# Optimization experiments

Hardware: AMD Instinct MI355X
Metric: run time of the kernel (lower is better)

The kernel has to match this reference:

```python
import jax, jax.numpy as jnp
import numpy as np

B, S, P, D, H = 2, 4096, 1024, 1024, 16  # batch, byte seq, patches, d_model, heads


def setup_inputs() -> dict:
    key = jax.random.key(0)
    ks = jax.random.split(key, 8)
    init = 0.02
    queries = jax.random.normal(ks[0], (B, S, D), dtype=jnp.float32)
    patch_representations = jax.random.normal(ks[1], (B, P, D), dtype=jnp.float32)
    patch_boundaries = jax.random.randint(ks[2], (B, S), 0, 2, dtype=jnp.int32)
    wq = jax.random.normal(ks[3], (D, D), dtype=jnp.float32) * init
    wk = jax.random.normal(ks[4], (D, D), dtype=jnp.float32) * init
    wv = jax.random.normal(ks[5], (D, D), dtype=jnp.float32) * init
    wo = jax.random.normal(ks[6], (D, D), dtype=jnp.float32) * init
    bq = jnp.zeros((D,), jnp.float32)
    bk = jnp.zeros((D,), jnp.float32)
    bv = jnp.zeros((D,), jnp.float32)
    bo = jnp.zeros((D,), jnp.float32)
    return {"queries": queries, "patch_representations": patch_representations,
            "patch_boundaries": patch_boundaries,
            "wq": wq, "wk": wk, "wv": wv, "wo": wo,
            "bq": bq, "bk": bk, "bv": bv, "bo": bo}


def reference(queries, patch_representations, patch_boundaries,
              wq, wk, wv, wo, bq, bk, bv, bo):
    b, s, d = queries.shape
    p = patch_representations.shape[1]
    h = H
    dh = d // h
    scale = 1.0 / jnp.sqrt(jnp.asarray(dh, queries.dtype))

    # in-projections (torch Linear: x @ W.T + b)
    q = (queries @ wq.T + bq).reshape(b, s, h, dh)
    k = (patch_representations @ wk.T + bk).reshape(b, p, h, dh)
    v = (patch_representations @ wv.T + bv).reshape(b, p, h, dh)

    # scores: [b, h, s, p]
    scores = jnp.einsum('bqhd,bkhd->bhqk', q, k) * scale

    # data-dependent patch-boundary mask: byte t may attend to patch j iff j <= cumsum(boundaries)[t]
    patch_idx = jnp.cumsum(patch_boundaries, axis=1)          # [b, s]
    mask = jnp.arange(p)[None, None, :] > patch_idx[:, :, None]  # [b, s, p], True = masked
    scores = jnp.where(mask[:, None, :, :], jnp.finfo(scores.dtype).min, scores)

    attn = jax.nn.softmax(scores, axis=-1)                    # dropout inactive (eval)
    out = jnp.einsum('bhqk,bkhd->bqhd', attn, v).reshape(b, s, d)
    return out @ wo.T + bo
```

## Files before the change

kernel.cpp:

```cpp
#include <hip/hip_runtime.h>


#define B_ 2
#define S_ 4096
#define P_ 1024
#define D_ 1024
#define H_ 16
#define DH_ 64

#define NCONV 14336

typedef __attribute__((ext_vector_type(8))) short short8;
typedef __attribute__((ext_vector_type(4))) float f32x4;
typedef __attribute__((ext_vector_type(16))) float f32x16;

#define KSCALE 0.18033688011112042f

#if __has_builtin(__builtin_amdgcn_exp2f)
#define EXP2(x) __builtin_amdgcn_exp2f(x)
#else
#define EXP2(x) exp2f(x)
#endif

static __device__ __forceinline__ unsigned short f2bf(float f) {
    unsigned int u = __float_as_uint(f);
    u += 0x7FFFu + ((u >> 16) & 1u);
    return (unsigned short)(u >> 16);
}

static __device__ __forceinline__ unsigned int cvtpk(float lo, float hi) {
    unsigned int r;
    asm("v_cvt_pk_bf16_f32 %0, %1, %2" : "=v"(r) : "v"(lo), "v"(hi));
    return r;
}

static __device__ __forceinline__ void plswap(unsigned int& x, unsigned int& y) {
    asm volatile("v_permlane32_swap_b32 %0, %1" : "+v"(x), "+v"(y));
}

static __device__ __forceinline__ void gll16(const unsigned short* g,
                                             const unsigned short* l) {
    __builtin_amdgcn_global_load_lds(
        (const __attribute__((address_space(1))) unsigned int*)g,
        (__attribute__((address_space(3))) unsigned int*)l,
        16, 0, 0);
}

__global__ __launch_bounds__(256) void xattn_convert_all(
    const float* __restrict__ queries, const float* __restrict__ patches,
    const float* __restrict__ wq, const float* __restrict__ wk,
    const float* __restrict__ wv, const float* __restrict__ wo,
    unsigned short* __restrict__ qb, unsigned short* __restrict__ pb,
    unsigned short* __restrict__ wqb, unsigned short* __restrict__ wkb,
    unsigned short* __restrict__ wvb, unsigned short* __restrict__ wob,
    const int* __restrict__ bounds, int* __restrict__ pidx) {
    if (blockIdx.x >= NCONV) {
        __shared__ int sdata[256];
        int b = blockIdx.x - NCONV;
        int t = threadIdx.x;
        const int* src = bounds + b * S_ + t * 16;
        int vals[16];
        int run = 0;
#pragma unroll
        for (int i = 0; i < 16; ++i) { run += src[i]; vals[i] = run; }
        sdata[t] = run;
        __syncthreads();
        for (int off = 1; off < 256; off <<= 1) {
            int v = (t >= off) ? sdata[t - off] : 0;
            __syncthreads();
            sdata[t] += v;
            __syncthreads();
        }
        int prefix = (t > 0) ? sdata[t - 1] : 0;
        int* dst = pidx + b * S_ + t * 16;
#pragma unroll
        for (int i = 0; i < 16; ++i) dst[i] = prefix + vals[i];
        return;
    }
    const int NQ = (B_ * S_ * D_) / 4;
    const int NP = (B_ * P_ * D_) / 4;
    const int NW = (D_ * D_) / 4;
    int i = blockIdx.x * 256 + threadIdx.x;
    const float* src;
    unsigned short* dst;
    int j;
    if (i < NQ) { src = queries; dst = qb; j = i; }
    else if (i < NQ + NP) { src = patches; dst = pb; j = i - NQ; }
    else {
        int k = i - NQ - NP;
        int wsel = k >> 18;
        j = k & (NW - 1);
        if (wsel == 0) { src = wq; dst = wqb; }
        else if (wsel == 1) { src = wk; dst = wkb; }
        else if (wsel == 2) { src = wv; dst = wvb; }
        else { src = wo; dst = wob; }
    }
    float4 v = ((const float4*)src)[j];
    ushort4 o;
    o.x = f2bf(v.x); o.y = f2bf(v.y); o.z = f2bf(v.z); o.w = f2bf(v.w);
    ((ushort4*)dst)[j] = o;
}

__global__ __launch_bounds__(512) void xattn_gemm_qkv(
    const unsigned short* __restrict__ qb, const unsigned short* __restrict__ pb,
    const unsigned short* __restrict__ wqb, const unsigned short* __restrict__ wkb,
    const unsigned short* __restrict__ wvb,
    const float* __restrict__ bq, const float* __restrict__ bk,
    const float* __restrict__ bv,
    unsigned short* __restrict__ Qout, unsigned short* __restrict__ Kout,
    unsigned short* __restrict__ Vout) {
    const int K = 1024, N = 1024;
    const int byy = blockIdx.y;
    int z, my;
    if (byy < 64)      { z = 0; my = byy; }
    else if (byy < 80) { z = 1; my = byy - 64; }
    else               { z = 2; my = byy - 80; }
    const unsigned short* A = (z == 0) ? qb : pb;
    const unsigned short* W = (z == 0) ? wqb : ((z == 1) ? wkb : wvb);
    const float* bias = (z == 0) ? bq : ((z == 1) ? bk : bv);

    __shared__ unsigned short As[2][128 * 32];
    __shared__ unsigned short Bs[2][256 * 32];

    const int m0 = my * 128;
    const int n0 = blockIdx.x * 256;
    const int t = threadIdx.x;
    const int w = t >> 6;
    const int l = t & 63;
    const int fr = l & 15, fq = l >> 4;
    const int wr = w >> 2, wc = w & 3;

    const int r0s = t >> 2;
    const int csw = ((t & 3) ^ ((t >> 3) & 3)) * 8;
    const unsigned short* Ap0 = A + (size_t)(m0 + r0s) * K + csw;
    const unsigned short* Wp0 = W + (size_t)(n0 + r0s) * K + csw;
    const unsigned short* Wp1 = W + (size_t)(n0 + 128 + r0s) * K + csw;

    const int gsw = (fq ^ ((fr >> 1) & 3)) * 8;

    f32x4 acc[4][4];
#pragma unroll
    for (int i = 0; i < 4; ++i)
#pragma unroll
        for (int j = 0; j < 4; ++j) acc[i][j] = (f32x4){0.f, 0.f, 0.f, 0.f};

    gll16(Ap0, &As[0][w * 512]);
    gll16(Wp0, &Bs[0][w * 512]);
    gll16(Wp1, &Bs[0][4096 + w * 512]);

    for (int kt = 0; kt < 32; ++kt) {
        __builtin_amdgcn_s_barrier();
        if (kt + 1 < 32) {
            const int nb = (kt + 1) & 1;
            const int ks = (kt + 1) * 32;
            gll16(Ap0 + ks, &As[nb][w * 512]);
            gll16(Wp0 + ks, &Bs[nb][w * 512]);
            gll16(Wp1 + ks, &Bs[nb][4096 + w * 512]);
            asm volatile("s_waitcnt vmcnt(3)" ::: "memory");
        } else {
            asm volatile("s_waitcnt vmcnt(0)" ::: "memory");
        }
        __builtin_amdgcn_sched_barrier(0);
        __builtin_amdgcn_s_barrier();

        const unsigned short* Ac = As[kt & 1];
        const unsigned short* Bc = Bs[kt & 1];
        short8 af[4], bf[4];
#pragma unroll
        for (int i = 0; i < 4; ++i)
            af[i] = *(const short8*)&Ac[(wr * 64 + i * 16 + fr) * 32 + gsw];
#pragma unroll
        for (int j = 0; j < 4; ++j)
            bf[j] = *(const short8*)&Bc[(wc * 64 + j * 16 + fr) * 32 + gsw];
        __builtin_amdgcn_s_setprio(1);
#pragma unroll
        for (int i = 0; i < 4; ++i)
#pragma unroll
            for (int j = 0; j < 4; ++j)
                acc[i][j] = __builtin_amdgcn_mfma_f32_16x16x32_bf16(af[i], bf[j], acc[i][j], 0, 0, 0);
        __builtin_amdgcn_s_setprio(0);
    }

#pragma unroll
    for (int j = 0; j < 4; ++j) {
        int n = n0 + wc * 64 + j * 16 + fr;
        float bvv = bias[n];
#pragma unroll
        for (int i = 0; i < 4; ++i) {
            int mbase = m0 + wr * 64 + i * 16 + fq * 4;
#pragma unroll
            for (int r = 0; r < 4; ++r) {
                float val = acc[i][j][r] + bvv;
                int m = mbase + r;
                if (z == 0) {
                    Qout[(size_t)m * N + n] = f2bf(val * KSCALE);
                } else if (z == 1) {
                    int bb = m >> 10, p = m & (P_ - 1);
                    int hh = n >> 6, k = n & 63;
                    size_t base = ((size_t)((bb * H_ + hh) * 16 + (p >> 6))) * 4096;
                    int off = (((p >> 5) & 1) * 4 + (k >> 4)) * 512 +
                              (((k >> 3) & 1) * 32 + (p & 31)) * 8 + (k & 7);
                    Kout[base + off] = f2bf(val);
                } else {
                    int bb = m >> 10, p = m & (P_ - 1);
                    int hh = n >> 6, d = n & 63;
                    size_t base = ((size_t)((bb * H_ + hh) * 16 + (p >> 6))) * 4096;
                    int off = ((d >> 5) * 4 + ((p >> 4) & 3)) * 512 +
                              ((((p >> 3) & 1) * 32) + (d & 31)) * 8 + (p & 7);
                    Vout[base + off] = f2bf(val);
                }
            }
        }
    }
}

__global__ __launch_bounds__(512) void xattn_gemm_o(
    const unsigned short* __restrict__ A,
    const unsigned short* __restrict__ W,
    const float* __restrict__ bias,
    float* __restrict__ Cout) {
    const int K = 1024, N = 1024;
    __shared__ unsigned short As[2][128 * 32];
    __shared__ unsigned short Bs[2][256 * 32];

    const int m0 = blockIdx.y * 128;
    const int n0 = blockIdx.x * 256;
    const int t = threadIdx.x;
    const int w = t >> 6;
    const int l = t & 63;
    const int fr = l & 15, fq = l >> 4;
    const int wr = w >> 2, wc = w & 3;

    const int r0s = t >> 2;
    const int csw = ((t & 3) ^ ((t >> 3) & 3)) * 8;
    const unsigned short* Ap0 = A + (size_t)(m0 + r0s) * K + csw;
    const unsigned short* Wp0 = W + (size_t)(n0 + r0s) * K + csw;
    const unsigned short* Wp1 = W + (size_t)(n0 + 128 + r0s) * K + csw;

    const int gsw = (fq ^ ((fr >> 1) & 3)) * 8;

    f32x4 acc[4][4];
#pragma unroll
    for (int i = 0; i < 4; ++i)
#pragma unroll
        for (int j = 0; j < 4; ++j) acc[i][j] = (f32x4){0.f, 0.f, 0.f, 0.f};

    gll16(Ap0, &As[0][w * 512]);
    gll16(Wp0, &Bs[0][w * 512]);
    gll16(Wp1, &Bs[0][4096 + w * 512]);

    for (int kt = 0; kt < 32; ++kt) {
        __builtin_amdgcn_s_barrier();
        if (kt + 1 < 32) {
            const int nb = (kt + 1) & 1;
            const int ks = (kt + 1) * 32;
            gll16(Ap0 + ks, &As[nb][w * 512]);
            gll16(Wp0 + ks, &Bs[nb][w * 512]);
            gll16(Wp1 + ks, &Bs[nb][4096 + w * 512]);
            asm volatile("s_waitcnt vmcnt(3)" ::: "memory");
        } else {
            asm volatile("s_waitcnt vmcnt(0)" ::: "memory");
        }
        __builtin_amdgcn_sched_barrier(0);
        __builtin_amdgcn_s_barrier();

        const unsigned short* Ac = As[kt & 1];
        const unsigned short* Bc = Bs[kt & 1];
        short8 af[4], bf[4];
#pragma unroll
        for (int i = 0; i < 4; ++i)
            af[i] = *(const short8*)&Ac[(wr * 64 + i * 16 + fr) * 32 + gsw];
#pragma unroll
        for (int j = 0; j < 4; ++j)
            bf[j] = *(const short8*)&Bc[(wc * 64 + j * 16 + fr) * 32 + gsw];
        __builtin_amdgcn_s_setprio(1);
#pragma unroll
        for (int i = 0; i < 4; ++i)
#pragma unroll
            for (int j = 0; j < 4; ++j)
                acc[i][j] = __builtin_amdgcn_mfma_f32_16x16x32_bf16(af[i], bf[j], acc[i][j], 0, 0, 0);
        __builtin_amdgcn_s_setprio(0);
    }

#pragma unroll
    for (int j = 0; j < 4; ++j) {
        int n = n0 + wc * 64 + j * 16 + fr;
        float bvv = bias[n];
#pragma unroll
        for (int i = 0; i < 4; ++i) {
            int mbase = m0 + wr * 64 + i * 16 + fq * 4;
#pragma unroll
            for (int r = 0; r < 4; ++r)
                Cout[(size_t)(mbase + r) * N + n] = acc[i][j][r] + bvv;
        }
    }
}

__global__ __launch_bounds__(512) void xattn_attn_mfma(
    const unsigned short* __restrict__ Qb,
    const unsigned short* __restrict__ Kf,
    const unsigned short* __restrict__ Vf,
    const int* __restrict__ pidx,
    unsigned short* __restrict__ Ob) {
    __shared__ unsigned short Ks[3][4096];
    __shared__ unsigned short Vs[3][4096];

    const int q0 = (31 - blockIdx.x) * 128;
    const int h = blockIdx.y;
    const int b = blockIdx.z;
    const int t = threadIdx.x;
    const int w = t >> 6, l = t & 63;
    const int lq = l & 31, lh = l >> 5;
    const int wq4 = w & 3, role = w >> 2;
    const int qw = q0 + wq4 * 32;

    const unsigned short* qrow =
        Qb + (size_t)(b * S_ + qw + lq) * D_ + h * DH_ + lh * 8;
    short8 qf[4];
#pragma unroll
    for (int ks = 0; ks < 4; ++ks) qf[ks] = *(const short8*)(qrow + ks * 16);

    const int prow = pidx[b * S_ + qw + lq];
    const int limit = pidx[b * S_ + q0 + 127];
    const int ntiles = (min(limit, P_ - 1) + 64) >> 6;
    const int nfull = (pidx[b * S_ + q0] + 1) >> 6;

    float l4[4] = {0.f, 0.f, 0.f, 0.f};
    f32x16 oacc[2] = {{}, {}};

    const unsigned short* kfb =
        Kf + (size_t)((b * H_ + h) * 16) * 4096 + w * 512 + l * 8;
    const unsigned short* vfb =
        Vf + (size_t)((b * H_ + h) * 16) * 4096 + w * 512 + l * 8;

    gll16(kfb, &Ks[0][w * 512]);
    gll16(vfb, &Vs[0][w * 512]);
    if (ntiles > 1) {
        gll16(kfb + 4096, &Ks[1][w * 512]);
        gll16(vfb + 4096, &Vs[1][w * 512]);
    }

    int cur = 0, nx2 = 2;
    for (int kt = 0; kt < ntiles; ++kt) {
        __builtin_amdgcn_s_barrier();
        if (kt + 2 < ntiles) {
            gll16(kfb + (size_t)(kt + 2) * 4096, &Ks[nx2][w * 512]);
            gll16(vfb + (size_t)(kt + 2) * 4096, &Vs[nx2][w * 512]);
            asm volatile("s_waitcnt vmcnt(4)" ::: "memory");
        } else if (kt + 1 < ntiles) {
            asm volatile("s_waitcnt vmcnt(2)" ::: "memory");
        } else {
            asm volatile("s_waitcnt vmcnt(0)" ::: "memory");
        }
        __builtin_amdgcn_sched_barrier(0);

        const unsigned short* Kc = Ks[cur];
        const unsigned short* Vc = Vs[cur];
        const int c0 = kt * 64;

        f32x16 sa = {};
        __builtin_amdgcn_s_setprio(1);
#pragma unroll
        for (int ks = 0; ks < 4; ++ks) {
            short8 kfr = *(const short8*)&Kc[(role * 4 + ks) * 512 + l * 8];
            sa = __builtin_amdgcn_mfma_f32_32x32x16_bf16(kfr, qf[ks], sa, 0, 0, 0);
        }
        __builtin_amdgcn_s_setprio(0);

        if (kt >= nfull) {
#pragma unroll
            for (int r = 0; r < 16; ++r) {
                const int pg = c0 + role * 32 + (r & 3) + 8 * (r >> 2) + 4 * lh;
                float p = EXP2(sa[r]);
                p = (pg > prow) ? 0.f : p;
                sa[r] = p;
                l4[r & 3] += p;
            }
        } else {
#pragma unroll
            for (int r = 0; r < 16; ++r) {
                float p = EXP2(sa[r]);
                sa[r] = p;
                l4[r & 3] += p;
            }
        }

        short8 pa[2];
#pragma unroll
        for (int psl = 0; psl < 2; ++psl) {
            const int rA = psl * 8;
            unsigned int X0 = cvtpk(sa[rA + 0], sa[rA + 1]);
            unsigned int Y0 = cvtpk(sa[rA + 4], sa[rA + 5]);
            unsigned int X1 = cvtpk(sa[rA + 2], sa[rA + 3]);
            unsigned int Y1 = cvtpk(sa[rA + 6], sa[rA + 7]);
            plswap(X0, Y0);
            plswap(X1, Y1);
            uint4 u = {X0, X1, Y0, Y1};
            pa[psl] = *(short8*)&u;
        }

        __builtin_amdgcn_s_setprio(1);
#pragma unroll
        for (int dt = 0; dt < 2; ++dt)
#pragma unroll
            for (int psl = 0; psl < 2; ++psl) {
                short8 vfr = *(const short8*)
                    &Vc[(dt * 4 + role * 2 + psl) * 512 + l * 8];
                oacc[dt] = __builtin_amdgcn_mfma_f32_32x32x16_bf16(pa[psl], vfr, oacc[dt], 0, 0, 0);
            }
        __builtin_amdgcn_s_setprio(0);

        cur = (cur == 2) ? 0 : cur + 1;
        nx2 = (nx2 == 2) ? 0 : nx2 + 1;
    }

    float lsum = (l4[0] + l4[1]) + (l4[2] + l4[3]);
    float* cf = (float*)&Ks[0][0];
    float* lf = (float*)&Vs[0][0];
    const int ci = wq4 * 64 + l;

    __builtin_amdgcn_s_barrier();
    if (role) {
#pragma unroll
        for (int r = 0; r < 16; ++r) cf[ci * 16 + r] = oacc[0][r];
        lf[ci] = lsum;
    }
    __builtin_amdgcn_s_barrier();
    if (!role) {
#pragma unroll
        for (int r = 0; r < 16; ++r) oacc[0][r] += cf[ci * 16 + r];
        lsum += lf[ci];
    }
    __builtin_amdgcn_s_barrier();
    if (role) {
#pragma unroll
        for (int r = 0; r < 16; ++r) cf[ci * 16 + r] = oacc[1][r];
    }
    __builtin_amdgcn_s_barrier();
    if (!role) {
#pragma unroll
        for (int r = 0; r < 16; ++r) oacc[1][r] += cf[ci * 16 + r];

        lsum += __shfl_xor(lsum, 32);
        const float inv = 1.0f / lsum;

        unsigned short* ob = Ob + (size_t)(b * S_ + qw) * D_ + h * DH_;
#pragma unroll
        for (int r = 0; r < 16; ++r) {
            const int qr = (r & 3) + 8 * (r >> 2) + 4 * lh;
            const float invr = __shfl(inv, qr);
            ob[(size_t)qr * D_ + lq] = f2bf(oacc[0][r] * invr);
            ob[(size_t)qr * D_ + 32 + lq] = f2bf(oacc[1][r] * invr);
        }
    }
}

extern "C" void kernel_launch(void* const* d_in, const int* in_sizes, int n_in,
                              void* d_out, int out_size, void* d_ws, size_t ws_size,
                              hipStream_t stream) {
    const float* queries = (const float*)d_in[0];
    const float* patches = (const float*)d_in[1];
    const int* bounds    = (const int*)d_in[2];
    const float* wq = (const float*)d_in[3];
    const float* wk = (const float*)d_in[4];
    const float* wv = (const float*)d_in[5];
    const float* wo = (const float*)d_in[6];
    const float* bq = (const float*)d_in[7];
    const float* bk = (const float*)d_in[8];
    const float* bv = (const float*)d_in[9];
    const float* bo = (const float*)d_in[10];
    float* out = (float*)d_out;

    char* ws = (char*)d_ws;
    unsigned short* qb    = (unsigned short*)(ws + 0);
    unsigned short* pb    = (unsigned short*)(ws + 16777216);
    unsigned short* wqb   = (unsigned short*)(ws + 20971520);
    unsigned short* wkb   = (unsigned short*)(ws + 23068672);
    unsigned short* wvb   = (unsigned short*)(ws + 25165824);
    unsigned short* wob   = (unsigned short*)(ws + 27262976);
    unsigned short* Qbf   = (unsigned short*)(ws + 29360128);
    unsigned short* Kfr   = (unsigned short*)(ws + 46137344);
    unsigned short* Vfr   = (unsigned short*)(ws + 50331648);
    unsigned short* attnb = (unsigned short*)(ws + 54525952);
    int* pidx             = (int*)(ws + 71303168);

    xattn_convert_all<<<dim3(NCONV + B_), 256, 0, stream>>>(
        queries, patches, wq, wk, wv, wo, qb, pb, wqb, wkb, wvb, wob,
        bounds, pidx);
    xattn_gemm_qkv<<<dim3(4, 96), 512, 0, stream>>>(
        qb, pb, wqb, wkb, wvb, bq, bk, bv, Qbf, Kfr, Vfr);
    xattn_attn_mfma<<<dim3(S_ / 128, H_, B_), 512, 0, stream>>>(
        Qbf, Kfr, Vfr, pidx, attnb);
    xattn_gemm_o<<<dim3(4, 64), 512, 0, stream>>>(attnb, wob, bo, out);
}
```

Baseline: 232.6 us.

## Process two KV tiles per iteration with double-buffered LDS in attention

The attention loop now handles pairs of 64-wide K/V tiles per iteration, using two 8192-element LDS buffers instead of three 4096-element ones. Interleaving the score MFMAs and the softmax/PV work for two tiles aims to raise instruction-level parallelism and halve the number of barriers and wait points. In exchange it uses more LDS and registers. When the tile count is odd it also computes one extra tile, which is fully masked to zero.

Result: slower. 251.0 us (+7.9%).

```diff
diff --git a/kernel.cpp b/kernel.cpp
--- a/kernel.cpp
+++ b/kernel.cpp
@@ -302,8 +302,8 @@
     const unsigned short* __restrict__ Vf,
     const int* __restrict__ pidx,
     unsigned short* __restrict__ Ob) {
-    __shared__ unsigned short Ks[3][4096];
-    __shared__ unsigned short Vs[3][4096];
+    __shared__ unsigned short Ks[2][8192];
+    __shared__ unsigned short Vs[2][8192];
 
     const int q0 = (31 - blockIdx.x) * 128;
     const int h = blockIdx.y;
@@ -324,6 +324,7 @@
     const int limit = pidx[b * S_ + q0 + 127];
     const int ntiles = (min(limit, P_ - 1) + 64) >> 6;
     const int nfull = (pidx[b * S_ + q0] + 1) >> 6;
+    const int npairs = (ntiles + 1) >> 1;
 
     float l4[4] = {0.f, 0.f, 0.f, 0.f};
     f32x16 oacc[2] = {{}, {}};
@@ -334,21 +335,22 @@
         Vf + (size_t)((b * H_ + h) * 16) * 4096 + w * 512 + l * 8;
 
     gll16(kfb, &Ks[0][w * 512]);
+    gll16(kfb + 4096, &Ks[0][4096 + w * 512]);
     gll16(vfb, &Vs[0][w * 512]);
-    if (ntiles > 1) {
-        gll16(kfb + 4096, &Ks[1][w * 512]);
-        gll16(vfb + 4096, &Vs[1][w * 512]);
-    }
-
-    int cur = 0, nx2 = 2;
-    for (int kt = 0; kt < ntiles; ++kt) {
+    gll16(vfb + 4096, &Vs[0][4096 + w * 512]);
+
+    for (int p = 0; p < npairs; ++p) {
+        const int cur = p & 1;
         __builtin_amdgcn_s_barrier();
-        if (kt + 2 < ntiles) {
-            gll16(kfb + (size_t)(kt + 2) * 4096, &Ks[nx2][w * 512]);
-            gll16(vfb + (size_t)(kt + 2) * 4096, &Vs[nx2][w * 512]);
+        if (p + 1 < npairs) {
+            const int nb = cur ^ 1;
+            const unsigned short* kn = kfb + (size_t)(2 * p + 2) * 4096;
+            const unsigned short* vn = vfb + (size_t)(2 * p + 2) * 4096;
+            gll16(kn, &Ks[nb][w * 512]);
+            gll16(kn + 4096, &Ks[nb][4096 + w * 512]);
+            gll16(vn, &Vs[nb][w * 512]);
+            gll16(vn + 4096, &Vs[nb][4096 + w * 512]);
             asm volatile("s_waitcnt vmcnt(4)" ::: "memory");
-        } else if (kt + 1 < ntiles) {
-            asm volatile("s_waitcnt vmcnt(2)" ::: "memory");
         } else {
             asm volatile("s_waitcnt vmcnt(0)" ::: "memory");
         }
@@ -356,36 +358,55 @@
 
         const unsigned short* Kc = Ks[cur];
         const unsigned short* Vc = Vs[cur];
-        const int c0 = kt * 64;
-
-        f32x16 sa = {};
+        const int ta = 2 * p, tb = 2 * p + 1;
+
+        f32x16 sa = {}, sb = {};
         __builtin_amdgcn_s_setprio(1);
 #pragma unroll
         for (int ks = 0; ks < 4; ++ks) {
-            short8 kfr = *(const short8*)&Kc[(role * 4 + ks) * 512 + l * 8];
-            sa = __builtin_amdgcn_mfma_f32_32x32x16_bf16(kfr, qf[ks], sa, 0, 0, 0);
+            short8 ka = *(const short8*)&Kc[(role * 4 + ks) * 512 + l * 8];
+            short8 kb = *(const short8*)&Kc[4096 + (role * 4 + ks) * 512 + l * 8];
+            sa = __builtin_amdgcn_mfma_f32_32x32x16_bf16(ka, qf[ks], sa, 0, 0, 0);
+            sb = __builtin_amdgcn_mfma_f32_32x32x16_bf16(kb, qf[ks], sb, 0, 0, 0);
         }
         __builtin_amdgcn_s_setprio(0);
 
-        if (kt >= nfull) {
+        if (ta >= nfull) {
 #pragma unroll
             for (int r = 0; r < 16; ++r) {
-                const int pg = c0 + role * 32 + (r & 3) + 8 * (r >> 2) + 4 * lh;
-                float p = EXP2(sa[r]);
-                p = (pg > prow) ? 0.f : p;
-                sa[r] = p;
-                l4[r & 3] += p;
+                const int pg = ta * 64 + role * 32 + (r & 3) + 8 * (r >> 2) + 4 * lh;
+                float pv = EXP2(sa[r]);
+                pv = (pg > prow) ? 0.f : pv;
+                sa[r] = pv;
+                l4[r & 3] += pv;
             }
         } else {
 #pragma unroll
             for (int r = 0; r < 16; ++r) {
-                float p = EXP2(sa[r]);
-                sa[r] = p;
-                l4[r & 3] += p;
+                float pv = EXP2(sa[r]);
+                sa[r] = pv;
+                l4[r & 3] += pv;
             }
         }
-
-        short8 pa[2];
+        if (tb >= nfull) {
+#pragma unroll
+            for (int r = 0; r < 16; ++r) {
+                const int pg = tb * 64 + role * 32 + (r & 3) + 8 * (r >> 2) + 4 * lh;
+                float pv = EXP2(sb[r]);
+                pv = (pg > prow) ? 0.f : pv;
+                sb[r] = pv;
+                l4[r & 3] += pv;
+            }
+        } else {
+#pragma unroll
+            for (int r = 0; r < 16; ++r) {
+                float pv = EXP2(sb[r]);
+                sb[r] = pv;
+                l4[r & 3] += pv;
+            }
+        }
+
+        short8 paa[2], pab[2];
 #pragma unroll
         for (int psl = 0; psl < 2; ++psl) {
             const int rA = psl * 8;
@@ -396,22 +417,33 @@
             plswap(X0, Y0);
             plswap(X1, Y1);
             uint4 u = {X0, X1, Y0, Y1};
-            pa[psl] = *(short8*)&u;
+            paa[psl] = *(short8*)&u;
+            unsigned int A0 = cvtpk(sb[rA + 0], sb[rA + 1]);
+            unsigned int B0 = cvtpk(sb[rA + 4], sb[rA + 5]);
+            unsigned int A1 = cvtpk(sb[rA + 2], sb[rA + 3]);
+            unsigned int B1 = cvtpk(sb[rA + 6], sb[rA + 7]);
+            plswap(A0, B0);
+            plswap(A1, B1);
+            uint4 v = {A0, A1, B0, B1};
+            pab[psl] = *(short8*)&v;
         }
 
         __builtin_amdgcn_s_setprio(1);
 #pragma unroll
-        for (int dt = 0; dt < 2; ++dt)
-#pragma unroll
-            for (int psl = 0; psl < 2; ++psl) {
-                short8 vfr = *(const short8*)
-                    &Vc[(dt * 4 + role * 2 + psl) * 512 + l * 8];
-                oacc[dt] = __builtin_amdgcn_mfma_f32_32x32x16_bf16(pa[psl], vfr, oacc[dt], 0, 0, 0);
-            }
+        for (int psl = 0; psl < 2; ++psl) {
+            short8 va0 = *(const short8*)&Vc[(0 * 4 + role * 2 + psl) * 512 + l * 8];
+            short8 va1 = *(const short8*)&Vc[(1 * 4 + role * 2 + psl) * 512 + l * 8];
+            oacc[0] = __builtin_amdgcn_mfma_f32_32x32x16_bf16(paa[psl], va0, oacc[0], 0, 0, 0);
+            oacc[1] = __builtin_amdgcn_mfma_f32_32x32x16_bf16(paa[psl], va1, oacc[1], 0, 0, 0);
+        }
+#pragma unroll
+        for (int psl = 0; psl < 2; ++psl) {
+            short8 vb0 = *(const short8*)&Vc[4096 + (0 * 4 + role * 2 + psl) * 512 + l * 8];
+            short8 vb1 = *(const short8*)&Vc[4096 + (1 * 4 + role * 2 + psl) * 512 + l * 8];
+            oacc[0] = __builtin_amdgcn_mfma_f32_32x32x16_bf16(pab[psl], vb0, oacc[0], 0, 0, 0);
+            oacc[1] = __builtin_amdgcn_mfma_f32_32x32x16_bf16(pab[psl], vb1, oacc[1], 0, 0, 0);
+        }
         __builtin_amdgcn_s_setprio(0);
-
-        cur = (cur == 2) ? 0 : cur + 1;
-        nx2 = (nx2 == 2) ? 0 : nx2 + 1;
     }
 
     float lsum = (l4[0] + l4[1]) + (l4[2] + l4[3]);
```
